# Kernel optimization log

Measured on AMD Instinct MI355X. Metric: run time of the kernel, lower is better.

## Reference

```python
import jax, jax.numpy as jnp
import numpy as np

TEMP = 0.1
EPS = 1e-8  # torch CosineSimilarity eps
B, C, T = 8, 256, 1024
M = 512    # masked positions per batch row (equal counts -> no padding branch)
K = 100    # negatives per masked position


def setup_inputs() -> dict:
    key = jax.random.key(0)
    k1, k2, k3 = jax.random.split(key, 3)
    context = jax.random.normal(k1, (B, C, T), dtype=jnp.float32)
    positive = jax.random.normal(k2, (B, C, T), dtype=jnp.float32)
    negatives = jax.random.normal(k3, (B, M, K, C), dtype=jnp.float32)
    # mask with exactly M True entries per row
    rng = np.random.default_rng(0)
    mask = np.zeros((B, T), dtype=bool)
    for b in range(B):
        mask[b, rng.permutation(T)[:M]] = True
    return {
        "context": context,
        "positive": positive,
        "negatives": negatives,
        "mask_indices": jnp.asarray(mask),
        "num_masked": M,
    }


def _cosine(a, b):
    # torch.nn.CosineSimilarity(dim=-1): dot / (max(|a|,eps) * max(|b|,eps))
    dot = jnp.sum(a * b, axis=-1)
    na = jnp.maximum(jnp.linalg.norm(a, axis=-1), EPS)
    nb = jnp.maximum(jnp.linalg.norm(b, axis=-1), EPS)
    return dot / (na * nb)


def reference(context, positive, negatives, mask_indices, num_masked):
    # [B,C,T] -> [B,T,C]
    ctx = jnp.transpose(context, (0, 2, 1))
    pos = jnp.transpose(positive, (0, 2, 1))
    # stable argsort puts masked positions first, preserving original order
    order = jnp.argsort(jnp.where(mask_indices, 0, 1), axis=1)  # [B,T]
    idx = order[:, :num_masked]                                 # [B,M]
    ctx_m = jnp.take_along_axis(ctx, idx[:, :, None], axis=1)   # [B,M,C]
    pos_m = jnp.take_along_axis(pos, idx[:, :, None], axis=1)   # [B,M,C]

    pos_sim = _cosine(ctx_m, pos_m)                    # [B,M]
    neg_sim = _cosine(ctx_m[:, :, None, :], negatives)  # [B,M,K]
    logits = jnp.concatenate([pos_sim[..., None], neg_sim], axis=-1) / TEMP  # [B,M,K+1]
    # cross-entropy with labels == 0, mean over B*M rows
    loss = jnp.mean(jax.nn.logsumexp(logits, axis=-1) - logits[..., 0])
    return loss
```

## Files before the change

kernel.cpp:

```cpp
#include <hip/hip_runtime.h>
#include <cstdint>

constexpr int Bb = 8;
constexpr int Cc = 256;
constexpr int Tt = 1024;
constexpr int Mm = 512;
constexpr int Kk = 100;
constexpr int GRID = (Bb * Mm) / 2;
#define EPSF 1e-8f
#define INV_TEMP 10.0f

typedef float vf4 __attribute__((ext_vector_type(4)));

__global__ __launch_bounds__(256)
void cl_main(const float* __restrict__ context,
             const float* __restrict__ positive,
             const float* __restrict__ negatives,
             const void*  __restrict__ mask,
             float*       __restrict__ lossbuf) {
    const int g    = blockIdx.x;
    const int bm0  = g * 2;
    const int b    = bm0 >> 9;
    const int m0   = bm0 & (Mm - 1);
    const int tid  = threadIdx.x;
    const int lane = tid & 63;
    const int wave = tid >> 6;
    const int q    = lane & 15;
    const int ks   = lane >> 4;

    __shared__ __align__(16) float ctx_s[2][Cc];
    __shared__ float redf[4][6];
    __shared__ int   redi[4][2];
    __shared__ int   scan_w[4];
    __shared__ float logits[2][Kk + 4];
    __shared__ int   t_sh[2];

    const uint8_t* p8  = (const uint8_t*)mask;
    const int32_t* p32 = (const int32_t*)mask;

    int c8 = 0, c32 = 0;
    #pragma unroll
    for (int j = 0; j < 4; ++j) {
        c8  += (p8 [j * 256 + tid] != 0);
        c32 += (p32[j * 256 + tid] != 0);
    }
    #pragma unroll
    for (int d = 32; d >= 1; d >>= 1) { c8 += __shfl_xor(c8, d); c32 += __shfl_xor(c32, d); }
    if (lane == 0) { redi[wave][0] = c8; redi[wave][1] = c32; }
    __syncthreads();
    const int tc8  = redi[0][0] + redi[1][0] + redi[2][0] + redi[3][0];
    const int tc32 = redi[0][1] + redi[1][1] + redi[2][1] + redi[3][1];
    const int esz  = (tc8 == Mm) ? 1 : ((tc32 == Mm) ? 4 : 8);

    int bits = 0;
    if (esz == 1) {
        const uint32_t w = *(const uint32_t*)(p8 + (size_t)b * Tt + tid * 4);
        bits = ((w & 0xffu)       ? 1 : 0) |
               ((w & 0xff00u)     ? 2 : 0) |
               ((w & 0xff0000u)   ? 4 : 0) |
               ((w & 0xff000000u) ? 8 : 0);
    } else if (esz == 4) {
        #pragma unroll
        for (int j = 0; j < 4; ++j)
            bits |= (p32[(size_t)b * Tt + tid * 4 + j] != 0) << j;
    } else {
        const int64_t* p64 = (const int64_t*)mask;
        #pragma unroll
        for (int j = 0; j < 4; ++j)
            bits |= (p64[(size_t)b * Tt + tid * 4 + j] != 0) << j;
    }
    const int cnt = __popc(bits);
    int incl = cnt;
    #pragma unroll
    for (int d = 1; d < 64; d <<= 1) { const int v = __shfl_up(incl, d); if (lane >= d) incl += v; }
    if (lane == 63) scan_w[wave] = incl;
    __syncthreads();
    int basec = 0;
    for (int w = 0; w < wave; ++w) basec += scan_w[w];
    incl += basec;
    const int excl = incl - cnt;
    #pragma unroll
    for (int sel = 0; sel < 2; ++sel) {
        const int mm = m0 + sel;
        if (excl <= mm && mm < incl) {
            int need = mm - excl;
            #pragma unroll
            for (int j = 0; j < 4; ++j) {
                if ((bits >> j) & 1) { if (need == 0) t_sh[sel] = tid * 4 + j; --need; }
            }
        }
    }
    __syncthreads();
    const int t0 = t_sh[0];
    const int t1 = t_sh[1];

    const float* crow = context  + (size_t)(b * Cc + tid) * Tt;
    const float* prow = positive + (size_t)(b * Cc + tid) * Tt;
    const float cv0 = crow[t0];
    const float pv0 = prow[t0];
    const float cv1 = crow[t1];
    const float pv1 = prow[t1];
    ctx_s[0][tid] = cv0;
    ctx_s[1][tid] = cv1;

    float s0 = cv0 * cv0, s1 = pv0 * pv0, s2 = cv0 * pv0;
    float s3 = cv1 * cv1, s4 = pv1 * pv1, s5 = cv1 * pv1;
    #pragma unroll
    for (int d = 32; d >= 1; d >>= 1) {
        s0 += __shfl_xor(s0, d); s1 += __shfl_xor(s1, d); s2 += __shfl_xor(s2, d);
        s3 += __shfl_xor(s3, d); s4 += __shfl_xor(s4, d); s5 += __shfl_xor(s5, d);
    }
    if (lane == 0) {
        redf[wave][0] = s0; redf[wave][1] = s1; redf[wave][2] = s2;
        redf[wave][3] = s3; redf[wave][4] = s4; redf[wave][5] = s5;
    }
    __syncthreads();

    const float4* c40 = (const float4*)ctx_s[0];
    const float4* c41 = (const float4*)ctx_s[1];
    float4 cr0[4], cr1[4];
    #pragma unroll
    for (int j = 0; j < 4; ++j) { cr0[j] = c40[j * 16 + q]; cr1[j] = c41[j * 16 + q]; }

    auto kloop = [&](const float4* cr, long long nbase, float* lrow) {
        #pragma unroll 2
        for (int it = 0; it < 7; ++it) {
            const int k = it * 16 + wave * 4 + ks;
            float dotp = 0.f, sq = 0.f;
            if (k < Kk) {
                const vf4* np4 = (const vf4*)(negatives + nbase + (long long)k * Cc);
                #pragma unroll
                for (int j = 0; j < 4; ++j) {
                    const vf4 nv = __builtin_nontemporal_load(np4 + j * 16 + q);
                    dotp += cr[j].x * nv.x + cr[j].y * nv.y + cr[j].z * nv.z + cr[j].w * nv.w;
                    sq   += nv.x * nv.x + nv.y * nv.y + nv.z * nv.z + nv.w * nv.w;
                }
            }
            #pragma unroll
            for (int d = 1; d <= 8; d <<= 1) {
                dotp += __shfl_xor(dotp, d);
                sq   += __shfl_xor(sq, d);
            }
            if (k < Kk && q == 0) {
                const float nb = fmaxf(sqrtf(sq), EPSF);
                lrow[1 + k] = dotp / nb;
            }
        }
    };

    auto lse = [&](const float* lrow, float na2, float np2, float dcp, int bm) {
        const float na = fmaxf(sqrtf(na2), EPSF);
        const float np = fmaxf(sqrtf(np2), EPSF);
        const float scale = INV_TEMP / na;
        const float a_raw = (lane == 0) ? (dcp / np) : lrow[lane];
        const float b_raw = (lane + 64 <= Kk) ? lrow[lane + 64] : -3e28f;
        const float a  = a_raw * scale;
        const float bb = b_raw * scale;
        float mx = fmaxf(a, bb);
        #pragma unroll
        for (int d = 32; d >= 1; d >>= 1) mx = fmaxf(mx, __shfl_xor(mx, d));
        float e = expf(a - mx) + expf(bb - mx);
        #pragma unroll
        for (int d = 32; d >= 1; d >>= 1) e += __shfl_xor(e, d);
        const float logit0 = __shfl(a, 0);
        if (lane == 0) lossbuf[bm] = mx + logf(e) - logit0;
    };

    const long long nbase0 = (long long)bm0 * Kk * Cc;

    kloop(cr0, nbase0, logits[0]);
    __syncthreads();

    if (wave == 0) {
        const float na2 = redf[0][0] + redf[1][0] + redf[2][0] + redf[3][0];
        const float np2 = redf[0][1] + redf[1][1] + redf[2][1] + redf[3][1];
        const float dcp = redf[0][2] + redf[1][2] + redf[2][2] + redf[3][2];
        lse(logits[0], na2, np2, dcp, bm0);
    }
    kloop(cr1, nbase0 + (long long)Kk * Cc, logits[1]);
    __syncthreads();

    if (wave == 0) {
        const float na2 = redf[0][3] + redf[1][3] + redf[2][3] + redf[3][3];
        const float np2 = redf[0][4] + redf[1][4] + redf[2][4] + redf[3][4];
        const float dcp = redf[0][5] + redf[1][5] + redf[2][5] + redf[3][5];
        lse(logits[1], na2, np2, dcp, bm0 + 1);
    }
}

__global__ __launch_bounds__(256)
void cl_reduce(const float* __restrict__ lossbuf, float* __restrict__ out) {
    const int tid = threadIdx.x;
    float s = 0.f;
    #pragma unroll
    for (int i = 0; i < 4; ++i) {
        const float4 v = *(const float4*)(lossbuf + tid * 16 + i * 4);
        s += (v.x + v.y) + (v.z + v.w);
    }
    #pragma unroll
    for (int d = 32; d >= 1; d >>= 1) s += __shfl_xor(s, d);
    __shared__ float ws[4];
    if ((tid & 63) == 0) ws[tid >> 6] = s;
    __syncthreads();
    if (tid == 0) out[0] = (ws[0] + ws[1] + ws[2] + ws[3]) * (1.0f / (Bb * Mm));
}

extern "C" void kernel_launch(void* const* d_in, const int* in_sizes, int n_in,
                              void* d_out, int out_size, void* d_ws, size_t ws_size,
                              hipStream_t stream) {
    const float* context   = (const float*)d_in[0];
    const float* positive  = (const float*)d_in[1];
    const float* negatives = (const float*)d_in[2];
    const void*  mask      = d_in[3];

    float* lossbuf = (float*)d_ws;

    cl_main<<<GRID, 256, 0, stream>>>(context, positive, negatives, mask, lossbuf);
    cl_reduce<<<1, 256, 0, stream>>>(lossbuf, (float*)d_out);
}
```

Measured before the change: 90.69 us.

## Prefetch first negative rows early and fuse both rows into one k-loop

Issues the first negatives load before the mask scan and gather, so that global-memory latency overlaps with the index computation. Merges the two per-row k-loops into a single 200-row loop over the contiguous negatives block, which removes the 7-iteration loops and their wasted k>=100 iterations and drops the intermediate barrier. Both LSE reductions now run at the end on waves 0 and 1 in parallel. In exchange, context values are read from shared memory on every iteration instead of being held in registers, and the prefetch keeps extra registers live across the mask phase.

```diff
diff --git a/kernel.cpp b/kernel.cpp
--- a/kernel.cpp
+++ b/kernel.cpp
@@ -27,13 +27,23 @@
     const int wave = tid >> 6;
     const int q    = lane & 15;
     const int ks   = lane >> 4;
+    const int g16  = wave * 4 + ks;
 
     __shared__ __align__(16) float ctx_s[2][Cc];
     __shared__ float redf[4][6];
     __shared__ int   redi[4][2];
     __shared__ int   scan_w[4];
-    __shared__ float logits[2][Kk + 4];
+    __shared__ float lraw[200];
     __shared__ int   t_sh[2];
+
+    const long long nbase = (long long)bm0 * Kk * Cc;
+
+    vf4 pre[4];
+    {
+        const vf4* np4 = (const vf4*)(negatives + nbase + (long long)g16 * Cc);
+        #pragma unroll
+        for (int j = 0; j < 4; ++j) pre[j] = __builtin_nontemporal_load(np4 + j * 16 + q);
+    }
 
     const uint8_t* p8  = (const uint8_t*)mask;
     const int32_t* p32 = (const int32_t*)mask;
@@ -116,44 +126,62 @@
     }
     __syncthreads();
 
-    const float4* c40 = (const float4*)ctx_s[0];
-    const float4* c41 = (const float4*)ctx_s[1];
-    float4 cr0[4], cr1[4];
-    #pragma unroll
-    for (int j = 0; j < 4; ++j) { cr0[j] = c40[j * 16 + q]; cr1[j] = c41[j * 16 + q]; }
-
-    auto kloop = [&](const float4* cr, long long nbase, float* lrow) {
-        #pragma unroll 2
-        for (int it = 0; it < 7; ++it) {
-            const int k = it * 16 + wave * 4 + ks;
-            float dotp = 0.f, sq = 0.f;
-            if (k < Kk) {
-                const vf4* np4 = (const vf4*)(negatives + nbase + (long long)k * Cc);
-                #pragma unroll
-                for (int j = 0; j < 4; ++j) {
-                    const vf4 nv = __builtin_nontemporal_load(np4 + j * 16 + q);
-                    dotp += cr[j].x * nv.x + cr[j].y * nv.y + cr[j].z * nv.z + cr[j].w * nv.w;
-                    sq   += nv.x * nv.x + nv.y * nv.y + nv.z * nv.z + nv.w * nv.w;
-                }
+    auto finish = [&](float dotp, float sq, int r) {
+        #pragma unroll
+        for (int d = 1; d <= 8; d <<= 1) {
+            dotp += __shfl_xor(dotp, d);
+            sq   += __shfl_xor(sq, d);
+        }
+        if (r < 200 && q == 0) {
+            const float nb = fmaxf(sqrtf(sq), EPSF);
+            lraw[r] = dotp / nb;
+        }
+    };
+
+    {
+        const vf4* cp = (const vf4*)ctx_s[0];
+        float dotp = 0.f, sq = 0.f;
+        #pragma unroll
+        for (int j = 0; j < 4; ++j) {
+            const vf4 c  = cp[j * 16 + q];
+            const vf4 nv = pre[j];
+            dotp += c.x * nv.x + c.y * nv.y + c.z * nv.z + c.w * nv.w;
+            sq   += nv.x * nv.x + nv.y * nv.y + nv.z * nv.z + nv.w * nv.w;
+        }
+        finish(dotp, sq, g16);
+    }
+
+    #pragma unroll 2
+    for (int it = 1; it < 13; ++it) {
+        const int r = it * 16 + g16;
+        const vf4* cp = (const vf4*)(ctx_s[0] + ((r >= 100) ? Cc : 0));
+        float dotp = 0.f, sq = 0.f;
+        if (r < 200) {
+            const vf4* np4 = (const vf4*)(negatives + nbase + (long long)r * Cc);
+            #pragma unroll
+            for (int j = 0; j < 4; ++j) {
+                const vf4 nv = __builtin_nontemporal_load(np4 + j * 16 + q);
+                const vf4 c  = cp[j * 16 + q];
+                dotp += c.x * nv.x + c.y * nv.y + c.z * nv.z + c.w * nv.w;
+                sq   += nv.x * nv.x + nv.y * nv.y + nv.z * nv.z + nv.w * nv.w;
             }
-            #pragma unroll
-            for (int d = 1; d <= 8; d <<= 1) {
-                dotp += __shfl_xor(dotp, d);
-                sq   += __shfl_xor(sq, d);
-            }
-            if (k < Kk && q == 0) {
-                const float nb = fmaxf(sqrtf(sq), EPSF);
-                lrow[1 + k] = dotp / nb;
-            }
-        }
-    };
-
-    auto lse = [&](const float* lrow, float na2, float np2, float dcp, int bm) {
+        }
+        finish(dotp, sq, r);
+    }
+    __syncthreads();
+
+    if (wave < 2) {
+        const int o = wave * 3;
+        const float na2 = redf[0][o]     + redf[1][o]     + redf[2][o]     + redf[3][o];
+        const float np2 = redf[0][o + 1] + redf[1][o + 1] + redf[2][o + 1] + redf[3][o + 1];
+        const float dcp = redf[0][o + 2] + redf[1][o + 2] + redf[2][o + 2] + redf[3][o + 2];
         const float na = fmaxf(sqrtf(na2), EPSF);
         const float np = fmaxf(sqrtf(np2), EPSF);
         const float scale = INV_TEMP / na;
-        const float a_raw = (lane == 0) ? (dcp / np) : lrow[lane];
-        const float b_raw = (lane + 64 <= Kk) ? lrow[lane + 64] : -3e28f;
+
+        const float* lr = lraw + wave * Kk;
+        const float a_raw = (lane == 0) ? (dcp / np) : lr[lane - 1];
+        const float b_raw = (lane + 64 <= Kk) ? lr[lane + 63] : -3e28f;
         const float a  = a_raw * scale;
         const float bb = b_raw * scale;
         float mx = fmaxf(a, bb);
@@ -163,28 +191,7 @@
         #pragma unroll
         for (int d = 32; d >= 1; d >>= 1) e += __shfl_xor(e, d);
         const float logit0 = __shfl(a, 0);
-        if (lane == 0) lossbuf[bm] = mx + logf(e) - logit0;
-    };
-
-    const long long nbase0 = (long long)bm0 * Kk * Cc;
-
-    kloop(cr0, nbase0, logits[0]);
-    __syncthreads();
-
-    if (wave == 0) {
-        const float na2 = redf[0][0] + redf[1][0] + redf[2][0] + redf[3][0];
-        const float np2 = redf[0][1] + redf[1][1] + redf[2][1] + redf[3][1];
-        const float dcp = redf[0][2] + redf[1][2] + redf[2][2] + redf[3][2];
-        lse(logits[0], na2, np2, dcp, bm0);
-    }
-    kloop(cr1, nbase0 + (long long)Kk * Cc, logits[1]);
-    __syncthreads();
-
-    if (wave == 0) {
-        const float na2 = redf[0][3] + redf[1][3] + redf[2][3] + redf[3][3];
-        const float np2 = redf[0][4] + redf[1][4] + redf[2][4] + redf[3][4];
-        const float dcp = redf[0][5] + redf[1][5] + redf[2][5] + redf[3][5];
-        lse(logits[1], na2, np2, dcp, bm0 + 1);
+        if (lane == 0) lossbuf[bm0 + wave] = mx + logf(e) - logit0;
     }
 }
 
```

Result: no change. 90.99 us (+0.3%).
